# Kernel tuning notes

Hardware: AMD Instinct MI355X
Metric: run time of the kernel (lower is better)

## Reference

```python
import jax, jax.numpy as jnp
import numpy as np

TOP_K = 8  # config.top_k


def setup_inputs() -> dict:
    key = jax.random.key(0)
    k1, k2 = jax.random.split(key)
    B, S, H, E = 4, 4096, 4096, 64
    x = jax.random.normal(k1, (B, S, H), dtype=jnp.float32)
    # nn.Linear(hidden_size, expert_num, bias=False) weight: [E, H]
    W = jax.random.normal(k2, (E, H), dtype=jnp.float32) / np.sqrt(H).astype(np.float32)
    return {"x": x, "W": W}


def reference(x, W):
    # gate linear: [B,S,H] @ [E,H]^T -> [B,S,E]
    logits = jnp.einsum('bsh,eh->bse', x, W)
    # top-k along experts
    topk_vals, indices = jax.lax.top_k(logits, TOP_K)  # [B,S,K]
    # scatter topk values into a -inf-filled tensor. Since the scattered src
    # values are exactly the logits at those indices, this equals masking.
    E = logits.shape[-1]
    mask = jax.nn.one_hot(indices, E, dtype=bool).any(axis=-2)  # [B,S,E]
    sparse_logits = jnp.where(mask, logits, -jnp.inf)
    sparse_probs = jax.nn.softmax(sparse_logits, axis=-1)  # [B,S,E]
    gate_logit = logits.reshape(-1, E)  # [B*S, E]
    return sparse_probs, indices, gate_logit
```

## Files before the change

### kernel.cpp

```cpp
#include <hip/hip_runtime.h>
#include <math.h>

#define H_DIM  4096
#define E_NUM  64
#define N_TOK  16384
#define TPB    64
#define KC     64
#define NCHUNK (H_DIM / KC)
#define TOPK   8

#define N_PROBS  (N_TOK * E_NUM)
#define N_IDX    (N_TOK * TOPK)
#define OFF_IDX  N_PROBS
#define OFF_GATE (N_PROBS + N_IDX)

#define XH 0
#define XM 1
#define XL 2
#define WH 3
#define WM 4
#define WL 5

typedef __attribute__((ext_vector_type(8)))  short short8;
typedef __attribute__((ext_vector_type(16))) float f32x16;

__device__ __forceinline__ unsigned short bf_split(float v, float& rem) {
  unsigned u  = __builtin_bit_cast(unsigned, v);
  unsigned hb = (u + 0x7FFFu + ((u >> 16) & 1u)) & 0xFFFF0000u;
  rem = v - __builtin_bit_cast(float, hb);
  return (unsigned short)(hb >> 16);
}
__device__ __forceinline__ unsigned short bf_rne(float v) {
  unsigned u = __builtin_bit_cast(unsigned, v);
  return (unsigned short)((u + 0x7FFFu + ((u >> 16) & 1u)) >> 16);
}

__global__ __launch_bounds__(256, 1)
void gating_kernel(const float* __restrict__ x, const float* __restrict__ W,
                   float* __restrict__ out) {
  __shared__ union {
    unsigned short tiles[2][6][64][64];
    float lg[TPB][E_NUM + 1];
  } u;

  const int tid  = threadIdx.x;
  const int tok0 = blockIdx.x * TPB;
  const int lane = tid & 63;
  const int wid  = tid >> 6;
  const int wm   = wid >> 1;
  const int wn   = wid & 1;
  const int l31  = lane & 31;
  const int arow = 32 * wm + l31;
  const int brow = 32 * wn + l31;
  const int kloff = 16 * (lane >> 5);

  const float* xg = x + (size_t)tok0 * H_DIM;

  auto sw = [&](int arr, int b, int row, int kbyte) -> void* {
    return (char*)(&u.tiles[b][arr][0][0]) +
           row * 128 + (kbyte ^ ((row & 7) << 4));
  };

  float4 xr[4], wr[4];

  auto gload = [&](int kb) {
#pragma unroll
    for (int p = 0; p < 4; ++p) {
      const int f4  = tid + 256 * p;
      const int row = f4 >> 4;
      const int kq  = f4 & 15;
      xr[p] = *(const float4*)(xg + (size_t)row * H_DIM + kb + 4 * kq);
      wr[p] = *(const float4*)(W  + (size_t)row * H_DIM + kb + 4 * kq);
    }
  };

  auto cvt_store = [&](const float4& v, int abase, int b, int row, int kbyte) {
    const float f[4] = {v.x, v.y, v.z, v.w};
    unsigned short h[4], m[4], l[4];
#pragma unroll
    for (int i = 0; i < 4; ++i) {
      float r1, r2;
      h[i] = bf_split(f[i], r1);
      m[i] = bf_split(r1, r2);
      l[i] = bf_rne(r2);
    }
    ushort4 hv = {h[0], h[1], h[2], h[3]};
    ushort4 mv = {m[0], m[1], m[2], m[3]};
    ushort4 lv = {l[0], l[1], l[2], l[3]};
    *(ushort4*)sw(abase + 0, b, row, kbyte) = hv;
    *(ushort4*)sw(abase + 1, b, row, kbyte) = mv;
    *(ushort4*)sw(abase + 2, b, row, kbyte) = lv;
  };

  auto sstore = [&](int b) {
#pragma unroll
    for (int p = 0; p < 4; ++p) {
      const int f4    = tid + 256 * p;
      const int row   = f4 >> 4;
      const int kbyte = (f4 & 15) * 8;
      cvt_store(xr[p], XH, b, row, kbyte);
      cvt_store(wr[p], WH, b, row, kbyte);
    }
  };

  gload(0);
  sstore(0);
  __syncthreads();

  f32x16 accA, accB;
  double accd[16];
#pragma unroll
  for (int r = 0; r < 16; ++r) { accA[r] = 0.f; accB[r] = 0.f; accd[r] = 0.0; }

  for (int c = 0; c < NCHUNK; ++c) {
    if (c + 1 < NCHUNK) gload((c + 1) * KC);
    const int b = c & 1;

#pragma unroll
    for (int kt = 0; kt < 4; ++kt) {
      const int kb = kt * 32 + kloff;
      const short8 ah = *(const short8*)sw(XH, b, arow, kb);
      const short8 am = *(const short8*)sw(XM, b, arow, kb);
      const short8 al = *(const short8*)sw(XL, b, arow, kb);
      const short8 bh = *(const short8*)sw(WH, b, brow, kb);
      const short8 bm = *(const short8*)sw(WM, b, brow, kb);
      const short8 bl = *(const short8*)sw(WL, b, brow, kb);
      accA = __builtin_amdgcn_mfma_f32_32x32x16_bf16(ah, bh, accA, 0, 0, 0);
      accB = __builtin_amdgcn_mfma_f32_32x32x16_bf16(am, bm, accB, 0, 0, 0);
      accA = __builtin_amdgcn_mfma_f32_32x32x16_bf16(am, bh, accA, 0, 0, 0);
      accB = __builtin_amdgcn_mfma_f32_32x32x16_bf16(ah, bm, accB, 0, 0, 0);
      accA = __builtin_amdgcn_mfma_f32_32x32x16_bf16(al, bh, accA, 0, 0, 0);
      accB = __builtin_amdgcn_mfma_f32_32x32x16_bf16(ah, bl, accB, 0, 0, 0);
    }

    if ((c & 3) == 3) {
#pragma unroll
      for (int r = 0; r < 16; ++r) {
        accd[r] += (double)accA[r] + (double)accB[r];
        accA[r] = 0.f; accB[r] = 0.f;
      }
    }

    if (c + 1 < NCHUNK) {
      sstore((c + 1) & 1);
      __syncthreads();
    }
  }

  __syncthreads();

  const int rb = 4 * (lane >> 5);
  float* gate = out + OFF_GATE;
#pragma unroll
  for (int q = 0; q < 4; ++q)
#pragma unroll
    for (int j = 0; j < 4; ++j) {
      const int reg   = 4 * q + j;
      const int row32 = j + 8 * q + rb;
      const float v   = (float)accd[reg];
      const int trow  = 32 * wm + row32;
      const int e     = 32 * wn + l31;
      gate[(size_t)(tok0 + trow) * E_NUM + e] = v;
      u.lg[trow][e] = v;
    }
  __syncthreads();

  if (tid < TPB) {
    const int t = tid;
    float vals[TOPK];
    int   idxs[TOPK];
#pragma unroll
    for (int p = 0; p < TOPK; ++p) {
      float best = -INFINITY;
      int   bi   = 0;
      for (int e = 0; e < E_NUM; ++e) {
        const float v = u.lg[t][e];
        if (v > best) { best = v; bi = e; }
      }
      vals[p] = best;
      idxs[p] = bi;
      u.lg[t][bi] = -INFINITY;
    }
    const float m = vals[0];
    float s = 0.f, pr[TOPK];
#pragma unroll
    for (int p = 0; p < TOPK; ++p) { pr[p] = __expf(vals[p] - m); s += pr[p]; }
    const float inv = 1.0f / s;
    for (int e = 0; e < E_NUM; ++e) u.lg[t][e] = 0.f;
#pragma unroll
    for (int p = 0; p < TOPK; ++p) u.lg[t][idxs[p]] = pr[p] * inv;

    float* oidx = out + OFF_IDX + (size_t)(tok0 + t) * TOPK;
#pragma unroll
    for (int p = 0; p < TOPK; ++p) oidx[p] = (float)idxs[p];
  }
  __syncthreads();

  float* oprob = out + (size_t)tok0 * E_NUM;
#pragma unroll
  for (int p = 0; p < 16; ++p) {
    const int f = tid + 256 * p;
    oprob[f] = u.lg[f >> 6][f & 63];
  }
}

extern "C" void kernel_launch(void* const* d_in, const int* in_sizes, int n_in,
                              void* d_out, int out_size, void* d_ws, size_t ws_size,
                              hipStream_t stream) {
  const float* x = (const float*)d_in[0];
  const float* W = (const float*)d_in[1];
  float* out = (float*)d_out;
  dim3 grid(N_TOK / TPB);
  dim3 block(256);
  gating_kernel<<<grid, block, 0, stream>>>(x, W, out);
}
```

Measured before the change: 405.9 us.

## Pre-split W into bf16x3 once and split K across two wave groups

A separate kernel converts W once into swizzled hi/mid/lo bf16 chunks in the workspace, so the gating kernel copies those bytes straight into shared memory instead of re-splitting W in every block. The block doubles to 512 threads: two groups of four waves each handle half of every K chunk, and their double-precision partial sums are reduced through shared memory at the end. This cuts per-block conversion ALU work and adds wave-level parallelism for latency hiding, at the cost of an extra launch, more shared-memory traffic and an extra reduction step.

```diff
diff --git a/kernel.cpp b/kernel.cpp
--- a/kernel.cpp
+++ b/kernel.cpp
@@ -14,12 +14,13 @@
 #define OFF_IDX  N_PROBS
 #define OFF_GATE (N_PROBS + N_IDX)
 
+#define W3_CHUNK_BYTES (3 * 64 * 64 * 2)
+#define W3_BYTES       (NCHUNK * W3_CHUNK_BYTES)
+
+
 #define XH 0
 #define XM 1
 #define XL 2
-#define WH 3
-#define WM 4
-#define WL 5
 
 typedef __attribute__((ext_vector_type(8)))  short short8;
 typedef __attribute__((ext_vector_type(16))) float f32x16;
@@ -36,45 +37,17 @@
 }
 
 __global__ __launch_bounds__(256, 1)
-void gating_kernel(const float* __restrict__ x, const float* __restrict__ W,
-                   float* __restrict__ out) {
-  __shared__ union {
-    unsigned short tiles[2][6][64][64];
-    float lg[TPB][E_NUM + 1];
-  } u;
-
-  const int tid  = threadIdx.x;
-  const int tok0 = blockIdx.x * TPB;
-  const int lane = tid & 63;
-  const int wid  = tid >> 6;
-  const int wm   = wid >> 1;
-  const int wn   = wid & 1;
-  const int l31  = lane & 31;
-  const int arow = 32 * wm + l31;
-  const int brow = 32 * wn + l31;
-  const int kloff = 16 * (lane >> 5);
-
-  const float* xg = x + (size_t)tok0 * H_DIM;
-
-  auto sw = [&](int arr, int b, int row, int kbyte) -> void* {
-    return (char*)(&u.tiles[b][arr][0][0]) +
-           row * 128 + (kbyte ^ ((row & 7) << 4));
-  };
-
-  float4 xr[4], wr[4];
-
-  auto gload = [&](int kb) {
-#pragma unroll
-    for (int p = 0; p < 4; ++p) {
-      const int f4  = tid + 256 * p;
-      const int row = f4 >> 4;
-      const int kq  = f4 & 15;
-      xr[p] = *(const float4*)(xg + (size_t)row * H_DIM + kb + 4 * kq);
-      wr[p] = *(const float4*)(W  + (size_t)row * H_DIM + kb + 4 * kq);
-    }
-  };
-
-  auto cvt_store = [&](const float4& v, int abase, int b, int row, int kbyte) {
+void wconv_kernel(const float* __restrict__ W, unsigned short* __restrict__ w3) {
+  const int c   = blockIdx.x;
+  const int t   = threadIdx.x;
+  const int r   = t >> 2;
+  const int kk0 = (t & 3) * 16;
+  const float* src = W + (size_t)r * H_DIM + c * KC + kk0;
+  char* dst = (char*)w3 + (size_t)c * W3_CHUNK_BYTES;
+  const int swz = (r & 7) << 4;
+#pragma unroll
+  for (int q = 0; q < 4; ++q) {
+    const float4 v = *(const float4*)(src + 4 * q);
     const float f[4] = {v.x, v.y, v.z, v.w};
     unsigned short h[4], m[4], l[4];
 #pragma unroll
@@ -84,26 +57,110 @@
       m[i] = bf_split(r1, r2);
       l[i] = bf_rne(r2);
     }
-    ushort4 hv = {h[0], h[1], h[2], h[3]};
-    ushort4 mv = {m[0], m[1], m[2], m[3]};
-    ushort4 lv = {l[0], l[1], l[2], l[3]};
-    *(ushort4*)sw(abase + 0, b, row, kbyte) = hv;
-    *(ushort4*)sw(abase + 1, b, row, kbyte) = mv;
-    *(ushort4*)sw(abase + 2, b, row, kbyte) = lv;
+    const int kb = 2 * (kk0 + 4 * q);
+    *(ushort4*)(dst + 0 * 8192 + r * 128 + (kb ^ swz)) = ushort4{h[0], h[1], h[2], h[3]};
+    *(ushort4*)(dst + 1 * 8192 + r * 128 + (kb ^ swz)) = ushort4{m[0], m[1], m[2], m[3]};
+    *(ushort4*)(dst + 2 * 8192 + r * 128 + (kb ^ swz)) = ushort4{l[0], l[1], l[2], l[3]};
+  }
+}
+
+template <bool PREW>
+__global__ __launch_bounds__(512, 2)
+void gating_kernel(const float* __restrict__ x, const float* __restrict__ W,
+                   float* __restrict__ out, const unsigned short* __restrict__ w3) {
+  __shared__ union {
+    struct { unsigned short xs[2][3][64][64]; unsigned short ws_[2][3][64][64]; } t;
+    struct { float pad[8192]; double dump[4][16][64]; } r;
+    float lg[TPB][E_NUM + 1];
+  } u;
+
+  const int tid  = threadIdx.x;
+  const int tok0 = blockIdx.x * TPB;
+  const int lane = tid & 63;
+  const int wid  = tid >> 6;
+  const int g    = wid >> 2;
+  const int sub  = wid & 3;
+  const int wm   = sub >> 1;
+  const int wn   = sub & 1;
+  const int l31  = lane & 31;
+  const int arow = 32 * wm + l31;
+  const int brow = 32 * wn + l31;
+  const int kloff = 16 * (lane >> 5);
+
+  const float* xg = x + (size_t)tok0 * H_DIM;
+  unsigned short* xbase = &u.t.xs[0][0][0][0];
+  unsigned short* wbase = &u.t.ws_[0][0][0][0];
+
+  auto sw = [](unsigned short* base, int row, int kbyte) -> void* {
+    return (char*)base + row * 128 + (kbyte ^ ((row & 7) << 4));
+  };
+
+  float4 xr[2], wr[2];
+  short8 wcp[3];
+
+  auto gloadX = [&](int kb) {
+#pragma unroll
+    for (int p = 0; p < 2; ++p) {
+      const int f4  = tid + 512 * p;
+      const int row = f4 >> 4;
+      const int kq  = f4 & 15;
+      xr[p] = *(const float4*)(xg + (size_t)row * H_DIM + kb + 4 * kq);
+    }
+  };
+  auto gloadW = [&](int c) {
+    if (PREW) {
+      const char* src = (const char*)w3 + (size_t)c * W3_CHUNK_BYTES + tid * 16;
+#pragma unroll
+      for (int s = 0; s < 3; ++s)
+        wcp[s] = *(const short8*)(src + s * 8192);
+    } else {
+      const int kb = c * KC;
+#pragma unroll
+      for (int p = 0; p < 2; ++p) {
+        const int f4  = tid + 512 * p;
+        const int row = f4 >> 4;
+        const int kq  = f4 & 15;
+        wr[p] = *(const float4*)(W + (size_t)row * H_DIM + kb + 4 * kq);
+      }
+    }
+  };
+
+  auto cvt_store = [&](const float4& v, unsigned short* base, int row, int kbyte) {
+    const float f[4] = {v.x, v.y, v.z, v.w};
+    unsigned short h[4], m[4], l[4];
+#pragma unroll
+    for (int i = 0; i < 4; ++i) {
+      float r1, r2;
+      h[i] = bf_split(f[i], r1);
+      m[i] = bf_split(r1, r2);
+      l[i] = bf_rne(r2);
+    }
+    *(ushort4*)sw(base + 0 * 4096, row, kbyte) = ushort4{h[0], h[1], h[2], h[3]};
+    *(ushort4*)sw(base + 1 * 4096, row, kbyte) = ushort4{m[0], m[1], m[2], m[3]};
+    *(ushort4*)sw(base + 2 * 4096, row, kbyte) = ushort4{l[0], l[1], l[2], l[3]};
   };
 
   auto sstore = [&](int b) {
-#pragma unroll
-    for (int p = 0; p < 4; ++p) {
-      const int f4    = tid + 256 * p;
+    unsigned short* xb = xbase + b * 3 * 4096;
+    unsigned short* wb = wbase + b * 3 * 4096;
+#pragma unroll
+    for (int p = 0; p < 2; ++p) {
+      const int f4    = tid + 512 * p;
       const int row   = f4 >> 4;
       const int kbyte = (f4 & 15) * 8;
-      cvt_store(xr[p], XH, b, row, kbyte);
-      cvt_store(wr[p], WH, b, row, kbyte);
-    }
-  };
-
-  gload(0);
+      cvt_store(xr[p], xb, row, kbyte);
+      if (!PREW) cvt_store(wr[p], wb, row, kbyte);
+    }
+    if (PREW) {
+      char* dst = (char*)wb + tid * 16;
+#pragma unroll
+      for (int s = 0; s < 3; ++s)
+        *(short8*)(dst + s * 8192) = wcp[s];
+    }
+  };
+
+  gloadX(0);
+  gloadW(0);
   sstore(0);
   __syncthreads();
 
@@ -113,18 +170,20 @@
   for (int r = 0; r < 16; ++r) { accA[r] = 0.f; accB[r] = 0.f; accd[r] = 0.0; }
 
   for (int c = 0; c < NCHUNK; ++c) {
-    if (c + 1 < NCHUNK) gload((c + 1) * KC);
+    if (c + 1 < NCHUNK) { gloadX((c + 1) * KC); gloadW(c + 1); }
     const int b = c & 1;
-
-#pragma unroll
-    for (int kt = 0; kt < 4; ++kt) {
-      const int kb = kt * 32 + kloff;
-      const short8 ah = *(const short8*)sw(XH, b, arow, kb);
-      const short8 am = *(const short8*)sw(XM, b, arow, kb);
-      const short8 al = *(const short8*)sw(XL, b, arow, kb);
-      const short8 bh = *(const short8*)sw(WH, b, brow, kb);
-      const short8 bm = *(const short8*)sw(WM, b, brow, kb);
-      const short8 bl = *(const short8*)sw(WL, b, brow, kb);
+    unsigned short* xb = xbase + b * 3 * 4096;
+    unsigned short* wb = wbase + b * 3 * 4096;
+
+#pragma unroll
+    for (int j = 0; j < 2; ++j) {
+      const int kb = (2 * g + j) * 32 + kloff;
+      const short8 ah = *(const short8*)sw(xb + 0 * 4096, arow, kb);
+      const short8 am = *(const short8*)sw(xb + 1 * 4096, arow, kb);
+      const short8 al = *(const short8*)sw(xb + 2 * 4096, arow, kb);
+      const short8 bh = *(const short8*)sw(wb + 0 * 4096, brow, kb);
+      const short8 bm = *(const short8*)sw(wb + 1 * 4096, brow, kb);
+      const short8 bl = *(const short8*)sw(wb + 2 * 4096, brow, kb);
       accA = __builtin_amdgcn_mfma_f32_32x32x16_bf16(ah, bh, accA, 0, 0, 0);
       accB = __builtin_amdgcn_mfma_f32_32x32x16_bf16(am, bm, accB, 0, 0, 0);
       accA = __builtin_amdgcn_mfma_f32_32x32x16_bf16(am, bh, accA, 0, 0, 0);
@@ -146,23 +205,30 @@
       __syncthreads();
     }
   }
-
-  __syncthreads();
-
-  const int rb = 4 * (lane >> 5);
-  float* gate = out + OFF_GATE;
-#pragma unroll
-  for (int q = 0; q < 4; ++q)
-#pragma unroll
-    for (int j = 0; j < 4; ++j) {
-      const int reg   = 4 * q + j;
-      const int row32 = j + 8 * q + rb;
-      const float v   = (float)accd[reg];
-      const int trow  = 32 * wm + row32;
-      const int e     = 32 * wn + l31;
-      gate[(size_t)(tok0 + trow) * E_NUM + e] = v;
-      u.lg[trow][e] = v;
-    }
+  __syncthreads();
+
+  if (g == 1) {
+#pragma unroll
+    for (int r = 0; r < 16; ++r) u.r.dump[sub][r][lane] = accd[r];
+  }
+  __syncthreads();
+
+  if (g == 0) {
+    const int rb = 4 * (lane >> 5);
+    float* gate = out + OFF_GATE;
+#pragma unroll
+    for (int q = 0; q < 4; ++q)
+#pragma unroll
+      for (int j = 0; j < 4; ++j) {
+        const int reg   = 4 * q + j;
+        const int row32 = j + 8 * q + rb;
+        const float v   = (float)(accd[reg] + u.r.dump[sub][reg][lane]);
+        const int trow  = 32 * wm + row32;
+        const int e     = 32 * wn + l31;
+        gate[(size_t)(tok0 + trow) * E_NUM + e] = v;
+        u.lg[trow][e] = v;
+      }
+  }
   __syncthreads();
 
   if (tid < TPB) {
@@ -198,8 +264,8 @@
 
   float* oprob = out + (size_t)tok0 * E_NUM;
 #pragma unroll
-  for (int p = 0; p < 16; ++p) {
-    const int f = tid + 256 * p;
+  for (int p = 0; p < 8; ++p) {
+    const int f = tid + 512 * p;
     oprob[f] = u.lg[f >> 6][f & 63];
   }
 }
@@ -210,7 +276,11 @@
   const float* x = (const float*)d_in[0];
   const float* W = (const float*)d_in[1];
   float* out = (float*)d_out;
-  dim3 grid(N_TOK / TPB);
-  dim3 block(256);
-  gating_kernel<<<grid, block, 0, stream>>>(x, W, out);
-}
+  if (ws_size >= (size_t)W3_BYTES && d_ws != nullptr) {
+    unsigned short* w3 = (unsigned short*)d_ws;
+    wconv_kernel<<<dim3(NCHUNK), dim3(256), 0, stream>>>(W, w3);
+    gating_kernel<true><<<dim3(N_TOK / TPB), dim3(512), 0, stream>>>(x, W, out, w3);
+  } else {
+    gating_kernel<false><<<dim3(N_TOK / TPB), dim3(512), 0, stream>>>(x, W, out, nullptr);
+  }
+}
```

After: 414.1 us. 1.02x slower.

## Switch to scaled fp16 hi/lo split with direct global-to-LDS fp32 staging

Applied to the files above, without the earlier changes.

Replaces the three-way bf16 split (6 MFMAs per k-step) with a scaled two-way fp16 split using four f16 MFMAs. The split now happens at fragment-read time from fp32 tiles in LDS. Tiles are staged with global_load_lds, which drops the register round trip and conversion on the store side and doubles the chunk size to 128. The aim is to cut MFMA count and staging overhead. In exchange the split is recomputed per wave from fp32 LDS data, and fp16 range depends on fixed scale factors, which could lose accuracy for inputs outside the expected range.

```diff
diff --git a/kernel.cpp b/kernel.cpp
--- a/kernel.cpp
+++ b/kernel.cpp
@@ -5,7 +5,7 @@
 #define E_NUM  64
 #define N_TOK  16384
 #define TPB    64
-#define KC     64
+#define KC     128
 #define NCHUNK (H_DIM / KC)
 #define TOPK   8
 
@@ -14,32 +14,20 @@
 #define OFF_IDX  N_PROBS
 #define OFF_GATE (N_PROBS + N_IDX)
 
-#define XH 0
-#define XM 1
-#define XL 2
-#define WH 3
-#define WM 4
-#define WL 5
 
-typedef __attribute__((ext_vector_type(8)))  short short8;
+typedef __attribute__((ext_vector_type(8))) __fp16 half8;
+typedef __attribute__((ext_vector_type(2))) __fp16 half2t;
 typedef __attribute__((ext_vector_type(16))) float f32x16;
 
-__device__ __forceinline__ unsigned short bf_split(float v, float& rem) {
-  unsigned u  = __builtin_bit_cast(unsigned, v);
-  unsigned hb = (u + 0x7FFFu + ((u >> 16) & 1u)) & 0xFFFF0000u;
-  rem = v - __builtin_bit_cast(float, hb);
-  return (unsigned short)(hb >> 16);
-}
-__device__ __forceinline__ unsigned short bf_rne(float v) {
-  unsigned u = __builtin_bit_cast(unsigned, v);
-  return (unsigned short)((u + 0x7FFFu + ((u >> 16) & 1u)) >> 16);
-}
+#define XSCALE 64.0f
+#define WSCALE 256.0f
+#define DESCALE (1.0 / 16384.0)
 
 __global__ __launch_bounds__(256, 1)
 void gating_kernel(const float* __restrict__ x, const float* __restrict__ W,
                    float* __restrict__ out) {
-  __shared__ union {
-    unsigned short tiles[2][6][64][64];
+  __shared__ union __align__(16) {
+    struct { float xs[2][64][KC]; float ws[2][64][KC]; } t;
     float lg[TPB][E_NUM + 1];
   } u;
 
@@ -52,102 +40,91 @@
   const int l31  = lane & 31;
   const int arow = 32 * wm + l31;
   const int brow = 32 * wn + l31;
-  const int kloff = 16 * (lane >> 5);
+  const int khalf = 32 * (lane >> 5);
 
   const float* xg = x + (size_t)tok0 * H_DIM;
 
-  auto sw = [&](int arr, int b, int row, int kbyte) -> void* {
-    return (char*)(&u.tiles[b][arr][0][0]) +
-           row * 128 + (kbyte ^ ((row & 7) << 4));
-  };
-
-  float4 xr[4], wr[4];
-
-  auto gload = [&](int kb) {
+  auto stage = [&](const float* gbase, float* lds, int cbyte) {
 #pragma unroll
-    for (int p = 0; p < 4; ++p) {
-      const int f4  = tid + 256 * p;
-      const int row = f4 >> 4;
-      const int kq  = f4 & 15;
-      xr[p] = *(const float4*)(xg + (size_t)row * H_DIM + kb + 4 * kq);
-      wr[p] = *(const float4*)(W  + (size_t)row * H_DIM + kb + 4 * kq);
+    for (int i = 0; i < 8; ++i) {
+      const int I   = wid * 8 + i;
+      const int row = 2 * I + (lane >> 5);
+      const int lin = (lane & 31) * 16;
+      const char* src = (const char*)(gbase + (size_t)row * H_DIM) + cbyte
+                        + (lin ^ ((row & 15) << 5));
+      __builtin_amdgcn_global_load_lds(
+          (const __attribute__((address_space(1))) unsigned int*)src,
+          (__attribute__((address_space(3))) unsigned int*)((char*)lds + I * 1024),
+          16, 0, 0);
     }
   };
 
-  auto cvt_store = [&](const float4& v, int abase, int b, int row, int kbyte) {
-    const float f[4] = {v.x, v.y, v.z, v.w};
-    unsigned short h[4], m[4], l[4];
+  auto fragp = [&](const float* base, int row, int kt) -> const float* {
+    const int kbyte = kt * 64 + khalf;
+    return (const float*)((const char*)base + row * 512
+                          + (kbyte ^ ((row & 15) << 5)));
+  };
+
+  auto split8 = [&](const float* p, float scale, half8& hi, half8& lo) {
+    const float4 v0 = ((const float4*)p)[0];
+    const float4 v1 = ((const float4*)p)[1];
+    float f[8] = {v0.x, v0.y, v0.z, v0.w, v1.x, v1.y, v1.z, v1.w};
+#pragma unroll
+    for (int i = 0; i < 8; ++i) f[i] *= scale;
 #pragma unroll
     for (int i = 0; i < 4; ++i) {
-      float r1, r2;
-      h[i] = bf_split(f[i], r1);
-      m[i] = bf_split(r1, r2);
-      l[i] = bf_rne(r2);
-    }
-    ushort4 hv = {h[0], h[1], h[2], h[3]};
-    ushort4 mv = {m[0], m[1], m[2], m[3]};
-    ushort4 lv = {l[0], l[1], l[2], l[3]};
-    *(ushort4*)sw(abase + 0, b, row, kbyte) = hv;
-    *(ushort4*)sw(abase + 1, b, row, kbyte) = mv;
-    *(ushort4*)sw(abase + 2, b, row, kbyte) = lv;
-  };
-
-  auto sstore = [&](int b) {
-#pragma unroll
-    for (int p = 0; p < 4; ++p) {
-      const int f4    = tid + 256 * p;
-      const int row   = f4 >> 4;
-      const int kbyte = (f4 & 15) * 8;
-      cvt_store(xr[p], XH, b, row, kbyte);
-      cvt_store(wr[p], WH, b, row, kbyte);
+      half2t h = __builtin_amdgcn_cvt_pkrtz(f[2 * i], f[2 * i + 1]);
+      const float r0 = f[2 * i]     - (float)h.x;
+      const float r1 = f[2 * i + 1] - (float)h.y;
+      half2t l = __builtin_amdgcn_cvt_pkrtz(r0, r1);
+      hi[2 * i] = h.x; hi[2 * i + 1] = h.y;
+      lo[2 * i] = l.x; lo[2 * i + 1] = l.y;
     }
   };
 
-  gload(0);
-  sstore(0);
+  stage(xg, &u.t.xs[0][0][0], 0);
+  stage(W,  &u.t.ws[0][0][0], 0);
   __syncthreads();
 
-  f32x16 accA, accB;
+  f32x16 aHH, aHL, aLH, aLL;
   double accd[16];
 #pragma unroll
-  for (int r = 0; r < 16; ++r) { accA[r] = 0.f; accB[r] = 0.f; accd[r] = 0.0; }
+  for (int r = 0; r < 16; ++r) {
+    aHH[r] = 0.f; aHL[r] = 0.f; aLH[r] = 0.f; aLL[r] = 0.f; accd[r] = 0.0;
+  }
 
   for (int c = 0; c < NCHUNK; ++c) {
-    if (c + 1 < NCHUNK) gload((c + 1) * KC);
     const int b = c & 1;
+    if (c + 1 < NCHUNK) {
+      const int cb = (c + 1) * KC * 4;
+      stage(xg, &u.t.xs[b ^ 1][0][0], cb);
+      stage(W,  &u.t.ws[b ^ 1][0][0], cb);
+    }
+    const float* xt = &u.t.xs[b][0][0];
+    const float* wt = &u.t.ws[b][0][0];
 
 #pragma unroll
-    for (int kt = 0; kt < 4; ++kt) {
-      const int kb = kt * 32 + kloff;
-      const short8 ah = *(const short8*)sw(XH, b, arow, kb);
-      const short8 am = *(const short8*)sw(XM, b, arow, kb);
-      const short8 al = *(const short8*)sw(XL, b, arow, kb);
-      const short8 bh = *(const short8*)sw(WH, b, brow, kb);
-      const short8 bm = *(const short8*)sw(WM, b, brow, kb);
-      const short8 bl = *(const short8*)sw(WL, b, brow, kb);
-      accA = __builtin_amdgcn_mfma_f32_32x32x16_bf16(ah, bh, accA, 0, 0, 0);
-      accB = __builtin_amdgcn_mfma_f32_32x32x16_bf16(am, bm, accB, 0, 0, 0);
-      accA = __builtin_amdgcn_mfma_f32_32x32x16_bf16(am, bh, accA, 0, 0, 0);
-      accB = __builtin_amdgcn_mfma_f32_32x32x16_bf16(ah, bm, accB, 0, 0, 0);
-      accA = __builtin_amdgcn_mfma_f32_32x32x16_bf16(al, bh, accA, 0, 0, 0);
-      accB = __builtin_amdgcn_mfma_f32_32x32x16_bf16(ah, bl, accB, 0, 0, 0);
+    for (int kt = 0; kt < KC / 16; ++kt) {
+      half8 ah, al, bh, bl;
+      split8(fragp(xt, arow, kt), XSCALE, ah, al);
+      split8(fragp(wt, brow, kt), WSCALE, bh, bl);
+      aHH = __builtin_amdgcn_mfma_f32_32x32x16_f16(ah, bh, aHH, 0, 0, 0);
+      aHL = __builtin_amdgcn_mfma_f32_32x32x16_f16(ah, bl, aHL, 0, 0, 0);
+      aLH = __builtin_amdgcn_mfma_f32_32x32x16_f16(al, bh, aLH, 0, 0, 0);
+      aLL = __builtin_amdgcn_mfma_f32_32x32x16_f16(al, bl, aLL, 0, 0, 0);
     }
 
-    if ((c & 3) == 3) {
+    if (c & 1) {
 #pragma unroll
       for (int r = 0; r < 16; ++r) {
-        accd[r] += (double)accA[r] + (double)accB[r];
-        accA[r] = 0.f; accB[r] = 0.f;
+        accd[r] += (double)aHH[r] + (double)aHL[r]
+                 + (double)aLH[r] + (double)aLL[r];
+        aHH[r] = 0.f; aHL[r] = 0.f; aLH[r] = 0.f; aLL[r] = 0.f;
       }
     }
 
-    if (c + 1 < NCHUNK) {
-      sstore((c + 1) & 1);
-      __syncthreads();
-    }
+    __syncthreads();
   }
-
-  __syncthreads();
 
   const int rb = 4 * (lane >> 5);
   float* gate = out + OFF_GATE;
@@ -157,7 +134,7 @@
     for (int j = 0; j < 4; ++j) {
       const int reg   = 4 * q + j;
       const int row32 = j + 8 * q + rb;
-      const float v   = (float)accd[reg];
+      const float v   = (float)(accd[reg] * DESCALE);
       const int trow  = 32 * wm + row32;
       const int e     = 32 * wn + l31;
       gate[(size_t)(tok0 + trow) * E_NUM + e] = v;
```

After: 437.4 us. 1.08x slower.
